# Kernel tuning notes

Measured on AMD Instinct MI355X. Metric: run time of the kernel, lower is better.

Reference implementation:

```python
import jax, jax.numpy as jnp
import numpy as np
from itertools import combinations

B, N, S = 2, 8192, 4096
NEIGHBOR_NUM, ANCHOR = 16, 4
IN_CH, TRANS_CH, OUT_CH = 64, 64, 128
INTRA = ANCHOR * (ANCHOR - 1) // 2            # 6 intra-anchor pairwise dists
GEN_CH = 2 * INTRA + ANCHOR * ANCHOR          # 28 = mlp_anchor_transition_fea input
BN_EPS = 1e-5


def index_points(points, idx):
    # points (B,N,C), idx (B,...) -> (B,...,C); torch index_points equivalent
    return jax.vmap(lambda p, i: p[i])(points, idx)


def index_dists(d, i, j):
    # d (B,N,N), i/j (B,...) same shape -> (B,...); torch index_points_dists equivalent
    return jax.vmap(lambda dd, a, b: dd[a, b])(d, i, j)


def knn_smallest(d, k):
    # k smallest along last dim, sorted ascending (self at position 0 since self-dist==0)
    neg, idx = jax.lax.top_k(-d, k)
    return -neg, idx


def gen_intra_anchor_dists(xyz_dists, nbr_dists, nbr_idx):
    # nbr_dists/nbr_idx: (B,P,ANCHOR); mirrors RotationInvariantDistFea.gen_intra_anchor_dists
    subs = [index_dists(xyz_dists, nbr_idx[:, :, pi], nbr_idx[:, :, pj])[:, :, None]
            for pi, pj in combinations(range(1, ANCHOR), 2)]
    return jnp.concatenate([nbr_dists[:, :, 1:]] + subs, axis=2)  # (B,P,INTRA)


def mlp_block(x, w, b, g, be):
    # Linear -> BatchNorm1d (eval mode, running mean 0 / var 1) -> LeakyReLU(0.2)
    x = x @ w + b
    x = x * (g / jnp.sqrt(jnp.asarray(1.0 + BN_EPS, x.dtype))) + be
    return jax.nn.leaky_relu(x, 0.2)


def forward_core(xyz, feature, w1, b1, g1, be1, w2, b2, g2, be2, w3, b3, g3, be3, sample_indexes):
    # --- RotationInvariantDistFea on full cloud (produces what msg carries in) ---
    sq = jnp.sum(xyz * xyz, -1)  # (B,N)
    d2 = sq[:, :, None] + sq[:, None, :] - 2.0 * jnp.einsum('bnc,bmc->bnm', xyz, xyz)
    xyz_dists = jnp.sqrt(jnp.maximum(d2, 1e-12))  # (B,N,N), clamp for grad safety at 0
    nbr_dists, nbr_idx = knn_smallest(xyz_dists, NEIGHBOR_NUM)
    intra_before = gen_intra_anchor_dists(xyz_dists, nbr_dists[:, :, :ANCHOR], nbr_idx[:, :, :ANCHOR])
    anchors_before = nbr_idx[:, :, :ANCHOR]  # (B,N,A) anchor idx in original index space

    # --- TransitionDownWithDistFea ---
    sampled_xyz = index_points(xyz, sample_indexes)          # (B,S,3)
    sampled_feature = index_points(feature, sample_indexes)  # (B,S,IN_CH)
    intra_before_s = index_points(intra_before, sample_indexes)    # (B,S,INTRA)
    anchors_before_s = index_points(anchors_before, sample_indexes)  # (B,S,A)

    Sn = sample_indexes.shape[1]
    # pairwise dists among sampled points, gathered from retained xyz_dists
    sd = index_dists(xyz_dists,
                     jnp.broadcast_to(sample_indexes[:, :, None], (B, Sn, Sn)),
                     jnp.broadcast_to(sample_indexes[:, None, :], (B, Sn, Sn)))
    s_nd, s_ni = knn_smallest(sd, ANCHOR)
    intra_after = gen_intra_anchor_dists(sd, s_nd, s_ni)  # (B,S,INTRA)
    anchors_after = jax.vmap(lambda s, i: s[i])(sample_indexes, s_ni)  # (B,S,A) orig idx

    # inter anchor dists: all A x A pairs between old and new anchors -> A^2 channels
    inter = index_dists(
        xyz_dists,
        jnp.broadcast_to(anchors_before_s[:, :, :, None], (B, Sn, ANCHOR, ANCHOR)),
        jnp.broadcast_to(anchors_after[:, :, None, :], (B, Sn, ANCHOR, ANCHOR)),
    ).reshape(B, Sn, ANCHOR * ANCHOR)

    trans = jnp.concatenate([intra_before_s, intra_after, inter], axis=2)  # (B,S,GEN_CH)
    trans = mlp_block(trans, w1, b1, g1, be1)
    trans = mlp_block(trans, w2, b2, g2, be2)
    out = mlp_block(jnp.concatenate([sampled_feature, trans], axis=2), w3, b3, g3, be3)
    return sampled_xyz, out


def setup_inputs() -> dict:
    key = jax.random.key(0)
    k = jax.random.split(key, 8)
    xyz = jax.random.normal(k[0], (B, N, 3), jnp.float32)
    feature = jax.random.normal(k[1], (B, N, IN_CH), jnp.float32)
    sample_indexes = jnp.stack([
        jnp.sort(jax.random.permutation(jax.random.fold_in(k[2], b), N)[:S])
        for b in range(B)]).astype(jnp.int32)  # uniform sampling w/o replacement

    def lin(kk, cin, cout):
        return jax.random.normal(kk, (cin, cout), jnp.float32) * (1.0 / np.sqrt(cin))

    zeros = lambda c: jnp.zeros((c,), jnp.float32)
    ones = lambda c: jnp.ones((c,), jnp.float32)
    return dict(
        xyz=xyz, feature=feature, sample_indexes=sample_indexes,
        w1=lin(k[3], GEN_CH, TRANS_CH), b1=zeros(TRANS_CH), g1=ones(TRANS_CH), be1=zeros(TRANS_CH),
        w2=lin(k[4], TRANS_CH, TRANS_CH), b2=zeros(TRANS_CH), g2=ones(TRANS_CH), be2=zeros(TRANS_CH),
        w3=lin(k[5], IN_CH + TRANS_CH, OUT_CH), b3=zeros(OUT_CH), g3=ones(OUT_CH), be3=zeros(OUT_CH),
    )


def reference(xyz, feature, sample_indexes, w1, b1, g1, be1, w2, b2, g2, be2, w3, b3, g3, be3):
    return forward_core(xyz, feature, w1, b1, g1, be1, w2, b2, g2, be2, w3, b3, g3, be3, sample_indexes)
```

## Files before the change

kernel.cpp:

```cpp
#include <hip/hip_runtime.h>
#include <math.h>

constexpr int cB = 2, cN = 8192, cS = 4096;
constexpr int cTR = 12;
constexpr int CAP = 96;
constexpr int QPB = 8;

typedef unsigned long long ull;

__device__ __forceinline__ float d2exact_rn(float qx, float qy, float qz, float qw,
                                            float cx, float cy, float cz, float cw) {
  float dot = __fadd_rn(__fadd_rn(__fmul_rn(qx, cx), __fmul_rn(qy, cy)), __fmul_rn(qz, cz));
  return __fsub_rn(__fadd_rn(qw, cw), __fmul_rn(2.0f, dot));
}
__device__ __forceinline__ float dist_rn4(float4 a, float4 b) {
  return sqrtf(fmaxf(d2exact_rn(a.x, a.y, a.z, a.w, b.x, b.y, b.z, b.w), 1e-12f));
}
__device__ __forceinline__ void ce64(ull& a, ull& b) {
  ull lo = a < b ? a : b;
  ull hi = a < b ? b : a;
  a = lo; b = hi;
}
__device__ __forceinline__ void cef(float& a, float& b) {
  float lo = fminf(a, b), hi = fmaxf(a, b);
  a = lo; b = hi;
}
__device__ __forceinline__ void top4_merge64(float& a0, float& a1, float& a2, float& a3) {
  #pragma unroll
  for (int off = 1; off < 64; off <<= 1) {
    float s0 = __shfl_xor(a0, off, 64), s1 = __shfl_xor(a1, off, 64);
    float s2 = __shfl_xor(a2, off, 64), s3 = __shfl_xor(a3, off, 64);
    float n0 = fminf(a0, s3), n1 = fminf(a1, s2), n2 = fminf(a2, s1), n3 = fminf(a3, s0);
    float t;
    t = fminf(n0, n2); n2 = fmaxf(n0, n2); n0 = t;
    t = fminf(n1, n3); n3 = fmaxf(n1, n3); n1 = t;
    t = fminf(n0, n1); n1 = fmaxf(n0, n1); n0 = t;
    t = fminf(n2, n3); n3 = fmaxf(n2, n3); n2 = t;
    a0 = n0; a1 = n1; a2 = n2; a3 = n3;
  }
}

__global__ __launch_bounds__(512) void pack_kernel(const float* __restrict__ xyz,
                                                   const int* __restrict__ smp,
                                                   float4* __restrict__ P,
                                                   float4* __restrict__ P2,
                                                   int* __restrict__ idxMap,
                                                   float* __restrict__ oxyz) {
  int t = blockIdx.x * 512 + threadIdx.x;
  if (t < cB * cN) {
    int b = t >> 13, n = t & (cN - 1);
    const float* p = xyz + t * 3;
    float x = p[0], y = p[1], z = p[2];
    float sq = __fadd_rn(__fadd_rn(__fmul_rn(x, x), __fmul_rn(y, y)), __fmul_rn(z, z));
    const int* sb = smp + b * cS;
    int lo = 0, hi = cS;
    while (lo < hi) { int mid = (lo + hi) >> 1; if (sb[mid] < n) lo = mid + 1; else hi = mid; }
    bool flg = (lo < cS) && (sb[lo] == n);
    P[t] = make_float4(x, y, z, sq);
    int pos = flg ? lo : (cS + n - lo);
    int gp = b * cN + pos;
    P2[gp] = make_float4(x, y, z, sq);
    idxMap[gp] = n;
  } else if (t < cB * cN + cB * cS) {
    int j = t - cB * cN;
    int b = j >> 12;
    const float* p = xyz + (b * cN + smp[j]) * 3;
    oxyz[j * 3 + 0] = p[0]; oxyz[j * 3 + 1] = p[1]; oxyz[j * 3 + 2] = p[2];
  }
}

#define KNN_FORQ(M) M(0) M(1) M(2) M(3) M(4) M(5) M(6) M(7)

__global__ __launch_bounds__(256, 4) void knn_kernel(const float4* __restrict__ P2,
                                                     const int* __restrict__ idxMap,
                                                     float* __restrict__ trans,
                                                     int* __restrict__ AB,
                                                     int* __restrict__ AA) {
  __shared__ int sPos[QPB][CAP];
  __shared__ int sCnt[QPB];
  __shared__ alignas(16) float tmpAll[QPB][256];
  __shared__ alignas(16) float gBuf[QPB];

  const int tid = threadIdx.x, wv = tid >> 6, lane = tid & 63;
  const int qbase = blockIdx.x * QPB;
  const int b = qbase >> 12;
  const int s0 = qbase & (cS - 1);
  const float4* Cb = P2 + b * cN;
  const int* im = idxMap + b * cN;
  const float INF = __uint_as_float(0x7f800000u);
  const float MARGIN = 2e-3f;

#define KNN_LOADQ(i) \
  const float4 q##i = Cb[s0 + i]; \
  const float qx##i = -2.0f * q##i.x, qy##i = -2.0f * q##i.y, qz##i = -2.0f * q##i.z;
  KNN_FORQ(KNN_LOADQ)
#undef KNN_LOADQ
  if (tid < QPB) sCnt[tid] = 0;

  float mn0 = INF, mn1 = INF, mn2 = INF, mn3 = INF;
  float mn4 = INF, mn5 = INF, mn6 = INF, mn7 = INF;
  #pragma unroll 4
  for (int k = 0; k < 16; k++) {
    float4 cp = Cb[k * 256 + tid];
#define KNN_AMIN(i) mn##i = fminf(mn##i, fmaf(qz##i, cp.z, fmaf(qy##i, cp.y, fmaf(qx##i, cp.x, cp.w))));
    KNN_FORQ(KNN_AMIN)
#undef KNN_AMIN
  }
#define KNN_WMIN(i) tmpAll[i][tid] = mn##i;
  KNN_FORQ(KNN_WMIN)
#undef KNN_WMIN
  __syncthreads();

  {
    const int qa = wv * 2;
    #pragma unroll
    for (int qq = 0; qq < 2; qq++) {
      float4 vq = *(const float4*)&tmpAll[qa + qq][lane * 4];
      float a0 = vq.x, a1 = vq.y, a2 = vq.z, a3 = vq.w;
      cef(a0, a1); cef(a2, a3); cef(a0, a2); cef(a1, a3); cef(a1, a2);
      top4_merge64(a0, a1, a2, a3);
      if (lane == 0) gBuf[qa + qq] = a3 + MARGIN;
    }
  }
  __syncthreads();
  const float g0 = gBuf[0], g1 = gBuf[1], g2 = gBuf[2], g3 = gBuf[3];
  const float g4 = gBuf[4], g5 = gBuf[5], g6 = gBuf[6], g7 = gBuf[7];

  #pragma unroll 2
  for (int k = 0; k < 32; k++) {
    int j = k * 256 + tid;
    float4 cp = Cb[j];
#define KNN_F(i) float f##i = fmaf(qz##i, cp.z, fmaf(qy##i, cp.y, fmaf(qx##i, cp.x, cp.w)));
    KNN_FORQ(KNN_F)
#undef KNN_F
    bool hit = (f0 <= g0) | (f1 <= g1) | (f2 <= g2) | (f3 <= g3)
             | (f4 <= g4) | (f5 <= g5) | (f6 <= g6) | (f7 <= g7);
    if (hit) {
#define KNN_PUSH(i) if (f##i <= g##i) { int s = atomicAdd(&sCnt[i], 1); if (s < CAP) sPos[i][s] = j; }
      KNN_FORQ(KNN_PUSH)
#undef KNN_PUSH
    }
  }
  __syncthreads();

  const ull KE = 0x7F800000FFFFFFFFull;
  #pragma unroll
  for (int qi = 0; qi < 2; qi++) {
    const int qloc = wv * 2 + qi;
    const float4 qv = Cb[s0 + qloc];
    #pragma unroll
    for (int mode = 0; mode < 2; mode++) {
      int cnt = sCnt[qloc]; cnt = cnt > CAP ? CAP : cnt;
      ull k0 = KE, k1 = KE;
      if (lane < cnt) {
        int pos = sPos[qloc][lane];
        if (mode == 0 || pos < cS) {
          float4 cp = Cb[pos];
          float fe = fmaxf(d2exact_rn(qv.x, qv.y, qv.z, qv.w, cp.x, cp.y, cp.z, cp.w), 1e-12f);
          unsigned idx = mode ? (unsigned)pos : (unsigned)im[pos];
          k0 = ((ull)__float_as_uint(fe) << 32) | idx;
        }
      }
      if (lane + 64 < cnt) {
        int pos = sPos[qloc][lane + 64];
        if (mode == 0 || pos < cS) {
          float4 cp = Cb[pos];
          float fe = fmaxf(d2exact_rn(qv.x, qv.y, qv.z, qv.w, cp.x, cp.y, cp.z, cp.w), 1e-12f);
          unsigned idx = mode ? (unsigned)pos : (unsigned)im[pos];
          k1 = ((ull)__float_as_uint(fe) << 32) | idx;
        }
      }
      if (k1 < k0) { ull t = k0; k0 = k1; k1 = t; }
      ull k2 = KE, k3 = KE;
      #pragma unroll
      for (int off = 1; off < 64; off <<= 1) {
        ull b0 = __shfl_xor(k0, off, 64), b1 = __shfl_xor(k1, off, 64);
        ull b2 = __shfl_xor(k2, off, 64), b3 = __shfl_xor(k3, off, 64);
        ull m0 = k0 < b3 ? k0 : b3;
        ull m1 = k1 < b2 ? k1 : b2;
        ull m2 = k2 < b1 ? k2 : b1;
        ull m3 = k3 < b0 ? k3 : b0;
        ce64(m0, m2); ce64(m1, m3); ce64(m0, m1); ce64(m2, m3);
        k0 = m0; k1 = m1; k2 = m2; k3 = m3;
      }
      if (lane == 0) {
        int wq = qbase + qloc;
        int i0 = (int)(unsigned)k0, i1 = (int)(unsigned)k1;
        int i2 = (int)(unsigned)k2, i3 = (int)(unsigned)k3;
        float e1 = sqrtf(__uint_as_float((unsigned)(k1 >> 32)));
        float e2 = sqrtf(__uint_as_float((unsigned)(k2 >> 32)));
        float e3 = sqrtf(__uint_as_float((unsigned)(k3 >> 32)));
        float* tr = trans + wq * cTR + (mode ? 6 : 0);
        tr[0] = e1; tr[1] = e2; tr[2] = e3;
        int* ao = (mode ? AA : AB) + wq * 4;
        if (mode) { i0 = im[i0]; i1 = im[i1]; i2 = im[i2]; i3 = im[i3]; }
        ao[0] = i0; ao[1] = i1; ao[2] = i2; ao[3] = i3;
      }
    }
  }
}

__global__ __launch_bounds__(64) void mlp_kernel(
    const float* __restrict__ TR, const float4* __restrict__ P,
    const int* __restrict__ AB, const int* __restrict__ AA,
    const float* __restrict__ feat, const int* __restrict__ smp,
    const float* __restrict__ w1, const float* __restrict__ b1,
    const float* __restrict__ g1, const float* __restrict__ be1,
    const float* __restrict__ w2, const float* __restrict__ b2,
    const float* __restrict__ g2, const float* __restrict__ be2,
    const float* __restrict__ w3, const float* __restrict__ b3,
    const float* __restrict__ g3, const float* __restrict__ be3,
    float* __restrict__ out) {
  __shared__ alignas(16) float tinT[28 * 4];
  __shared__ alignas(16) float act1T[64 * 4];
  __shared__ alignas(16) float act2T[128 * 4];

  const int lane = threadIdx.x;
  const int r0 = blockIdx.x * 4;
  const int b = r0 >> 12;
  const float inv = 1.0f / sqrtf(1.0f + 1e-5f);

  float pb1 = b1[lane], pg1 = g1[lane] * inv, pe1 = be1[lane];
  float pb2 = b2[lane], pg2 = g2[lane] * inv, pe2 = be2[lane];
  float pb3a = b3[lane],      pg3a = g3[lane] * inv,      pe3a = be3[lane];
  float pb3b = b3[lane + 64], pg3b = g3[lane + 64] * inv, pe3b = be3[lane + 64];

  {
    const float* fb = feat + (size_t)b * cN * 64;
    float4 v;
    v.x = fb[smp[r0 + 0] * 64 + lane];
    v.y = fb[smp[r0 + 1] * 64 + lane];
    v.z = fb[smp[r0 + 2] * 64 + lane];
    v.w = fb[smp[r0 + 3] * 64 + lane];
    *(float4*)&act2T[lane * 4] = v;
  }
  {
    const float4* Pb = P + b * cN;
    #pragma unroll
    for (int t = 0; t < 2; t++) {
      int idx = t * 64 + lane;
      if (idx < 112) {
        int r = idx & 3, ch = idx >> 2;
        float v;
        if (ch < 3) {
          v = TR[(r0 + r) * cTR + ch];
        } else if (ch < 6) {
          int pi = (ch == 3) ? 1 : 1 + (ch - 4), pj = (ch == 3) ? 2 : 3;
          if (ch == 5) { pi = 2; pj = 3; }
          v = dist_rn4(Pb[AB[(r0 + r) * 4 + pi]], Pb[AB[(r0 + r) * 4 + pj]]);
        } else if (ch < 9) {
          v = TR[(r0 + r) * cTR + ch];
        } else if (ch < 12) {
          int cc = ch - 9;
          int pi = (cc == 0) ? 1 : ((cc == 1) ? 1 : 2);
          int pj = (cc == 0) ? 2 : 3;
          v = dist_rn4(Pb[AA[(r0 + r) * 4 + pi]], Pb[AA[(r0 + r) * 4 + pj]]);
        } else {
          int cc = ch - 12;
          int gi = AB[(r0 + r) * 4 + (cc >> 2)];
          int gj = AA[(r0 + r) * 4 + (cc & 3)];
          v = dist_rn4(Pb[gi], Pb[gj]);
        }
        tinT[ch * 4 + r] = v;
      }
    }
  }
  __syncthreads();

  {
    float4 acc = make_float4(pb1, pb1, pb1, pb1);
    #pragma unroll 4
    for (int k = 0; k < 28; k++) {
      float w = w1[k * 64 + lane];
      float4 a = *(const float4*)&tinT[k * 4];
      acc.x = fmaf(a.x, w, acc.x); acc.y = fmaf(a.y, w, acc.y);
      acc.z = fmaf(a.z, w, acc.z); acc.w = fmaf(a.w, w, acc.w);
    }
    float4 o;
    o.x = fmaf(acc.x, pg1, pe1); o.y = fmaf(acc.y, pg1, pe1);
    o.z = fmaf(acc.z, pg1, pe1); o.w = fmaf(acc.w, pg1, pe1);
    o.x = o.x >= 0.0f ? o.x : 0.2f * o.x; o.y = o.y >= 0.0f ? o.y : 0.2f * o.y;
    o.z = o.z >= 0.0f ? o.z : 0.2f * o.z; o.w = o.w >= 0.0f ? o.w : 0.2f * o.w;
    __syncthreads();
    *(float4*)&act1T[lane * 4] = o;
  }
  __syncthreads();
  {
    float4 acc = make_float4(pb2, pb2, pb2, pb2);
    #pragma unroll 8
    for (int k = 0; k < 64; k++) {
      float w = w2[k * 64 + lane];
      float4 a = *(const float4*)&act1T[k * 4];
      acc.x = fmaf(a.x, w, acc.x); acc.y = fmaf(a.y, w, acc.y);
      acc.z = fmaf(a.z, w, acc.z); acc.w = fmaf(a.w, w, acc.w);
    }
    float4 o;
    o.x = fmaf(acc.x, pg2, pe2); o.y = fmaf(acc.y, pg2, pe2);
    o.z = fmaf(acc.z, pg2, pe2); o.w = fmaf(acc.w, pg2, pe2);
    o.x = o.x >= 0.0f ? o.x : 0.2f * o.x; o.y = o.y >= 0.0f ? o.y : 0.2f * o.y;
    o.z = o.z >= 0.0f ? o.z : 0.2f * o.z; o.w = o.w >= 0.0f ? o.w : 0.2f * o.w;
    *(float4*)&act2T[(64 + lane) * 4] = o;
  }
  __syncthreads();
  {
    float4 aA = make_float4(pb3a, pb3a, pb3a, pb3a);
    float4 aB = make_float4(pb3b, pb3b, pb3b, pb3b);
    #pragma unroll 8
    for (int k = 0; k < 128; k++) {
      float wA = w3[k * 128 + lane];
      float wB = w3[k * 128 + 64 + lane];
      float4 a = *(const float4*)&act2T[k * 4];
      aA.x = fmaf(a.x, wA, aA.x); aA.y = fmaf(a.y, wA, aA.y);
      aA.z = fmaf(a.z, wA, aA.z); aA.w = fmaf(a.w, wA, aA.w);
      aB.x = fmaf(a.x, wB, aB.x); aB.y = fmaf(a.y, wB, aB.y);
      aB.z = fmaf(a.z, wB, aB.z); aB.w = fmaf(a.w, wB, aB.w);
    }
    float rA0 = aA.x, rA1 = aA.y, rA2 = aA.z, rA3 = aA.w;
    float rB0 = aB.x, rB1 = aB.y, rB2 = aB.z, rB3 = aB.w;
    float xA, xB;
    xA = fmaf(rA0, pg3a, pe3a); xB = fmaf(rB0, pg3b, pe3b);
    xA = xA >= 0.0f ? xA : 0.2f * xA; xB = xB >= 0.0f ? xB : 0.2f * xB;
    out[(r0 + 0) * 128 + lane] = xA; out[(r0 + 0) * 128 + 64 + lane] = xB;
    xA = fmaf(rA1, pg3a, pe3a); xB = fmaf(rB1, pg3b, pe3b);
    xA = xA >= 0.0f ? xA : 0.2f * xA; xB = xB >= 0.0f ? xB : 0.2f * xB;
    out[(r0 + 1) * 128 + lane] = xA; out[(r0 + 1) * 128 + 64 + lane] = xB;
    xA = fmaf(rA2, pg3a, pe3a); xB = fmaf(rB2, pg3b, pe3b);
    xA = xA >= 0.0f ? xA : 0.2f * xA; xB = xB >= 0.0f ? xB : 0.2f * xB;
    out[(r0 + 2) * 128 + lane] = xA; out[(r0 + 2) * 128 + 64 + lane] = xB;
    xA = fmaf(rA3, pg3a, pe3a); xB = fmaf(rB3, pg3b, pe3b);
    xA = xA >= 0.0f ? xA : 0.2f * xA; xB = xB >= 0.0f ? xB : 0.2f * xB;
    out[(r0 + 3) * 128 + lane] = xA; out[(r0 + 3) * 128 + 64 + lane] = xB;
  }
}

extern "C" void kernel_launch(void* const* d_in, const int* in_sizes, int n_in,
                              void* d_out, int out_size, void* d_ws, size_t ws_size,
                              hipStream_t stream) {
  const float* xyz  = (const float*)d_in[0];
  const float* feat = (const float*)d_in[1];
  const int*   smp  = (const int*)d_in[2];
  const float* w1   = (const float*)d_in[3];
  const float* b1   = (const float*)d_in[4];
  const float* g1   = (const float*)d_in[5];
  const float* be1  = (const float*)d_in[6];
  const float* w2   = (const float*)d_in[7];
  const float* b2   = (const float*)d_in[8];
  const float* g2   = (const float*)d_in[9];
  const float* be2  = (const float*)d_in[10];
  const float* w3   = (const float*)d_in[11];
  const float* b3   = (const float*)d_in[12];
  const float* g3   = (const float*)d_in[13];
  const float* be3  = (const float*)d_in[14];
  float* out = (float*)d_out;

  char* ws = (char*)d_ws;
  float4* P      = (float4*)(ws);
  float4* P2     = (float4*)(ws + 262144);
  int*    idxMap = (int*)(ws + 524288);
  float*  TR     = (float*)(ws + 589824);
  int*    AB     = (int*)(ws + 983040);
  int*    AA     = (int*)(ws + 1114112);

  pack_kernel<<<48, 512, 0, stream>>>(xyz, smp, P, P2, idxMap, out);
  knn_kernel<<<cB * cS / QPB, 256, 0, stream>>>(P2, idxMap, TR, AB, AA);
  mlp_kernel<<<2048, 64, 0, stream>>>(TR, P, AB, AA, feat, smp,
                                      w1, b1, g1, be1, w2, b2, g2, be2,
                                      w3, b3, g3, be3, out + cB * cS * 3);
}
```

Baseline: 138.2 us.

## Split KNN candidate scan across two blocks per query group and add merge kernel

Each group of 8 queries is now handled by two blocks. Each block scans half of the candidate points and writes a partial top-4 as packed keys to a workspace buffer. The sampled-subset mode runs only in the first half, because sampled points are packed into positions below S. A new merge kernel combines the two partial top-4 lists, then computes the distances and writes the anchor indices. The aim is to double the grid and give the GPU more parallelism and latency hiding, at the cost of one extra launch, extra global traffic, and some duplicated threshold work per block.

```diff
diff --git a/kernel.cpp b/kernel.cpp
--- a/kernel.cpp
+++ b/kernel.cpp
@@ -73,22 +73,24 @@
 
 __global__ __launch_bounds__(256, 4) void knn_kernel(const float4* __restrict__ P2,
                                                      const int* __restrict__ idxMap,
-                                                     float* __restrict__ trans,
-                                                     int* __restrict__ AB,
-                                                     int* __restrict__ AA) {
+                                                     ull* __restrict__ PT) {
   __shared__ int sPos[QPB][CAP];
   __shared__ int sCnt[QPB];
   __shared__ alignas(16) float tmpAll[QPB][256];
   __shared__ alignas(16) float gBuf[QPB];
 
   const int tid = threadIdx.x, wv = tid >> 6, lane = tid & 63;
-  const int qbase = blockIdx.x * QPB;
+  const int blk = blockIdx.x;
+  const int half = blk & 1;
+  const int qbase = (blk >> 1) * QPB;
   const int b = qbase >> 12;
   const int s0 = qbase & (cS - 1);
   const float4* Cb = P2 + b * cN;
   const int* im = idxMap + b * cN;
   const float INF = __uint_as_float(0x7f800000u);
   const float MARGIN = 2e-3f;
+  const int jA = half * 2048;
+  const int jB = half * 4096;
 
 #define KNN_LOADQ(i) \
   const float4 q##i = Cb[s0 + i]; \
@@ -100,8 +102,8 @@
   float mn0 = INF, mn1 = INF, mn2 = INF, mn3 = INF;
   float mn4 = INF, mn5 = INF, mn6 = INF, mn7 = INF;
   #pragma unroll 4
-  for (int k = 0; k < 16; k++) {
-    float4 cp = Cb[k * 256 + tid];
+  for (int k = 0; k < 8; k++) {
+    float4 cp = Cb[jA + k * 256 + tid];
 #define KNN_AMIN(i) mn##i = fminf(mn##i, fmaf(qz##i, cp.z, fmaf(qy##i, cp.y, fmaf(qx##i, cp.x, cp.w))));
     KNN_FORQ(KNN_AMIN)
 #undef KNN_AMIN
@@ -127,8 +129,8 @@
   const float g4 = gBuf[4], g5 = gBuf[5], g6 = gBuf[6], g7 = gBuf[7];
 
   #pragma unroll 2
-  for (int k = 0; k < 32; k++) {
-    int j = k * 256 + tid;
+  for (int k = 0; k < 16; k++) {
+    int j = jB + k * 256 + tid;
     float4 cp = Cb[j];
 #define KNN_F(i) float f##i = fmaf(qz##i, cp.z, fmaf(qy##i, cp.y, fmaf(qx##i, cp.x, cp.w)));
     KNN_FORQ(KNN_F)
@@ -144,12 +146,12 @@
   __syncthreads();
 
   const ull KE = 0x7F800000FFFFFFFFull;
+  const int nm = half ? 1 : 2;
   #pragma unroll
   for (int qi = 0; qi < 2; qi++) {
     const int qloc = wv * 2 + qi;
     const float4 qv = Cb[s0 + qloc];
-    #pragma unroll
-    for (int mode = 0; mode < 2; mode++) {
+    for (int mode = 0; mode < nm; mode++) {
       int cnt = sCnt[qloc]; cnt = cnt > CAP ? CAP : cnt;
       ull k0 = KE, k1 = KE;
       if (lane < cnt) {
@@ -184,19 +186,46 @@
         k0 = m0; k1 = m1; k2 = m2; k3 = m3;
       }
       if (lane == 0) {
-        int wq = qbase + qloc;
-        int i0 = (int)(unsigned)k0, i1 = (int)(unsigned)k1;
-        int i2 = (int)(unsigned)k2, i3 = (int)(unsigned)k3;
-        float e1 = sqrtf(__uint_as_float((unsigned)(k1 >> 32)));
-        float e2 = sqrtf(__uint_as_float((unsigned)(k2 >> 32)));
-        float e3 = sqrtf(__uint_as_float((unsigned)(k3 >> 32)));
-        float* tr = trans + wq * cTR + (mode ? 6 : 0);
-        tr[0] = e1; tr[1] = e2; tr[2] = e3;
-        int* ao = (mode ? AA : AB) + wq * 4;
-        if (mode) { i0 = im[i0]; i1 = im[i1]; i2 = im[i2]; i3 = im[i3]; }
-        ao[0] = i0; ao[1] = i1; ao[2] = i2; ao[3] = i3;
+        ull* pt = PT + (size_t)(qbase + qloc) * 12 + (mode ? 8 : (half ? 4 : 0));
+        pt[0] = k0; pt[1] = k1; pt[2] = k2; pt[3] = k3;
       }
     }
+  }
+}
+
+__global__ __launch_bounds__(256) void merge_kernel(const ull* __restrict__ PT,
+                                                    const int* __restrict__ idxMap,
+                                                    float* __restrict__ trans,
+                                                    int* __restrict__ AB,
+                                                    int* __restrict__ AA) {
+  int t = blockIdx.x * 256 + threadIdx.x;
+  if (t >= cB * cS) return;
+  const int b = t >> 12;
+  const int* im = idxMap + b * cN;
+  const ull* p = PT + (size_t)t * 12;
+
+  ull v0 = p[0], v1 = p[1], v2 = p[2], v3 = p[3];
+  ull v4 = p[7], v5 = p[6], v6 = p[5], v7 = p[4];
+  ce64(v0, v4); ce64(v1, v5); ce64(v2, v6); ce64(v3, v7);
+  ce64(v0, v2); ce64(v1, v3); ce64(v0, v1); ce64(v2, v3);
+  {
+    float* tr = trans + t * cTR;
+    tr[0] = sqrtf(__uint_as_float((unsigned)(v1 >> 32)));
+    tr[1] = sqrtf(__uint_as_float((unsigned)(v2 >> 32)));
+    tr[2] = sqrtf(__uint_as_float((unsigned)(v3 >> 32)));
+    int* ao = AB + t * 4;
+    ao[0] = (int)(unsigned)v0; ao[1] = (int)(unsigned)v1;
+    ao[2] = (int)(unsigned)v2; ao[3] = (int)(unsigned)v3;
+  }
+  {
+    ull w0 = p[8], w1 = p[9], w2 = p[10], w3 = p[11];
+    float* tr = trans + t * cTR + 6;
+    tr[0] = sqrtf(__uint_as_float((unsigned)(w1 >> 32)));
+    tr[1] = sqrtf(__uint_as_float((unsigned)(w2 >> 32)));
+    tr[2] = sqrtf(__uint_as_float((unsigned)(w3 >> 32)));
+    int* ao = AA + t * 4;
+    ao[0] = im[(unsigned)w0]; ao[1] = im[(unsigned)w1];
+    ao[2] = im[(unsigned)w2]; ao[3] = im[(unsigned)w3];
   }
 }
 
@@ -360,9 +389,11 @@
   float*  TR     = (float*)(ws + 589824);
   int*    AB     = (int*)(ws + 983040);
   int*    AA     = (int*)(ws + 1114112);
+  ull*    PT     = (ull*)(ws + 1245184);
 
   pack_kernel<<<48, 512, 0, stream>>>(xyz, smp, P, P2, idxMap, out);
-  knn_kernel<<<cB * cS / QPB, 256, 0, stream>>>(P2, idxMap, TR, AB, AA);
+  knn_kernel<<<cB * cS / QPB * 2, 256, 0, stream>>>(P2, idxMap, PT);
+  merge_kernel<<<cB * cS / 256, 256, 0, stream>>>(PT, idxMap, TR, AB, AA);
   mlp_kernel<<<2048, 64, 0, stream>>>(TR, P, AB, AA, feat, smp,
                                       w1, b1, g1, be1, w2, b2, g2, be2,
                                       w3, b3, g3, be3, out + cB * cS * 3);
```

After: 148.5 us. +7.5%, slower.
